# Optimization experiments

Hardware: AMD Instinct MI355X
Metric: run time of the kernel (lower is better)

## Reference

```python
import jax, jax.numpy as jnp
import numpy as np

N, E, G = 30000, 240000, 1000
F, H = 78, 10            # in-features, GAT heads
HID = F * H              # 780
NEG_SLOPE = 0.2


def setup_inputs() -> dict:
    key = jax.random.key(0)
    ks = jax.random.split(key, 12)
    x = jax.random.normal(ks[0], (N, F), dtype=jnp.float32)
    edge_index = jax.random.randint(ks[1], (2, E), 0, N, dtype=jnp.int32)
    batch = jnp.sort(jax.random.randint(ks[2], (N,), 0, G, dtype=jnp.int32))
    def lin(k, fan_in, shape):
        return (jax.random.normal(k, shape, dtype=jnp.float32)
                / jnp.sqrt(jnp.float32(fan_in)))
    return {
        "x": x,
        "edge_index": edge_index,
        "batch": batch,
        "W_gat": lin(ks[3], F, (F, HID)),          # GATConv lin weight
        "att_src": lin(ks[4], F, (H, F)),          # GAT attention vectors
        "att_dst": lin(ks[5], F, (H, F)),
        "b_gat": jnp.zeros((HID,), jnp.float32),
        "W_gcn": lin(ks[6], HID, (HID, HID)),
        "b_gcn": jnp.zeros((HID,), jnp.float32),
        "W1": lin(ks[7], 2 * HID, (2 * HID, 1500)),
        "b1": jnp.zeros((1500,), jnp.float32),
        "W2": lin(ks[8], 1500, (1500, 128)),
        "b2": jnp.zeros((128,), jnp.float32),
    }


def _with_self_loops(edge_index):
    loop = jnp.arange(N, dtype=edge_index.dtype)
    src = jnp.concatenate([edge_index[0], loop])
    dst = jnp.concatenate([edge_index[1], loop])
    return src, dst


def reference(x, edge_index, batch, W_gat, att_src, att_dst, b_gat,
              W_gcn, b_gcn, W1, b1, W2, b2):
    src, dst = _with_self_loops(edge_index)  # [E+N]

    # ---- GATConv(78 -> 78, heads=10, concat) ----
    h = (x @ W_gat).reshape(N, H, F)                       # [N,H,F]
    a_src = jnp.einsum('nhf,hf->nh', h, att_src)           # [N,H]
    a_dst = jnp.einsum('nhf,hf->nh', h, att_dst)
    e = jax.nn.leaky_relu(a_src[src] + a_dst[dst], NEG_SLOPE)  # [Et,H]
    # segment softmax over incoming edges of each dst node
    e_max = jax.ops.segment_max(e, dst, num_segments=N)
    e_exp = jnp.exp(e - e_max[dst])
    denom = jax.ops.segment_sum(e_exp, dst, num_segments=N)
    alpha = e_exp / denom[dst]                             # [Et,H]
    msg = h[src] * alpha[:, :, None]                       # [Et,H,F]
    out = jax.ops.segment_sum(msg, dst, num_segments=N).reshape(N, HID) + b_gat
    out = jax.nn.relu(out)

    # ---- GCNConv(780 -> 780), symmetric norm with self loops ----
    h2 = out @ W_gcn                                       # [N,HID]
    deg = jax.ops.segment_sum(jnp.ones_like(dst, jnp.float32), dst,
                              num_segments=N)
    dinv = jax.lax.rsqrt(jnp.maximum(deg, 1.0))
    norm = dinv[src] * dinv[dst]                           # [Et]
    out2 = jax.ops.segment_sum(norm[:, None] * h2[src], dst,
                               num_segments=N) + b_gcn
    out2 = jax.nn.relu(out2)

    # ---- global mean / max pool over molecules ----
    counts = jax.ops.segment_sum(jnp.ones((N,), jnp.float32), batch,
                                 num_segments=G)
    gsum = jax.ops.segment_sum(out2, batch, num_segments=G)
    gmean = gsum / jnp.maximum(counts, 1.0)[:, None]
    gmax = jax.ops.segment_max(out2, batch, num_segments=G)
    gmax = jnp.where(counts[:, None] > 0, gmax, 0.0)
    pooled = jnp.concatenate([gmean, gmax], axis=1)        # [G, 1560]

    # ---- MLP head (dropout = identity at eval) ----
    hidfc = jax.nn.relu(pooled @ W1 + b1)
    return hidfc @ W2 + b2                                 # [G, 128]
```

## Files before the change

kernel.cpp:

```cpp
#include <hip/hip_runtime.h>

#define NN 30000
#define EE 240000
#define ET 270000
#define GG 1000
#define NH 10
#define FF 78
#define HID 780
#define NEG_SLOPE 0.2f

#define LD_H 784
#define KP_GCN 800
#define NP_HID 896
#define KP_X 96
#define LD_Z 960
#define MP_N 30080
#define KP_P 1600
#define NP_W1 1536
#define LD_FC 1536
#define MP_G 1024

#define MT 128
#define NT 128
#define NBLK 30
#define EB 4

#define C_X   (MP_N * KP_X)
#define C_WE  (NH * 128 * 96)
#define C_WC  (NP_HID * KP_GCN)
#define C_W1  (NP_W1 * KP_P)
#define C_W2  (128 * LD_FC)
#define C_PB  KP_GCN
#define C_WS  (FF * 2 * NH)
#define C_IN  NN
#define C_TOT (C_X + C_WE + C_WC + C_W1 + C_W2 + C_PB + C_WS + C_IN)

typedef __bf16 bf16_8 __attribute__((ext_vector_type(8)));
typedef float f32x4 __attribute__((ext_vector_type(4)));

__device__ __forceinline__ void async_copy16(const void* g, void* l) {
  __builtin_amdgcn_global_load_lds(
      (const __attribute__((address_space(1))) void*)g,
      (__attribute__((address_space(3))) void*)l, 16, 0, 0);
}

__device__ __forceinline__ float bf2f(unsigned int bits) {
  return __uint_as_float(bits << 16);
}

template <bool OUT_BF, int KBC, bool DBUF>
__global__ __launch_bounds__(256) void mfma_gemm(
    const __bf16* __restrict__ A, const __bf16* __restrict__ BT,
    float* __restrict__ Cf, __bf16* __restrict__ Cb,
    const float* __restrict__ bias, int M, int Kp, int Nout, int ldc,
    int relu, int rp, int nct, int mtiles) {
  constexpr int NST = KBC / 32;
  constexpr int TST = KBC / 16;
  constexpr int STAGEB = (KBC / 8) * MT * 8 * 2;
  __shared__ char smem[32768];
  int rt, ct;
  if (rp > 0) {
    int bid = blockIdx.x;
    int p = bid & 7, s = bid >> 3;
    int q = s / nct;
    rt = p * rp + q;
    ct = s - q * nct;
    if (rt >= mtiles) return;
  } else {
    rt = blockIdx.y; ct = blockIdx.x;
  }
  int row0 = rt * MT, col0 = ct * NT;
  int tid = threadIdx.x;
  int lane = tid & 63, wave = tid >> 6;
  int wm = (wave & 1) * 64, wn = (wave >> 1) * 64;
  int l15 = lane & 15, quad = lane >> 4;
  f32x4 acc[4][4] = {};

  auto stage = [&](int k0, int buf) {
    char* baseA = smem + (DBUF ? buf * 2 * STAGEB : 0);
    char* baseB = baseA + STAGEB;
    for (int t = 0; t < TST; t++) {
      int base = t * 256 + wave * 64;
      int s = base + lane;
      int kc = s >> 7, r = s & 127;
      async_copy16(A + (size_t)(row0 + r) * Kp + k0 + kc * 8,
                   baseA + (size_t)base * 16);
    }
    for (int t = 0; t < TST; t++) {
      int base = t * 256 + wave * 64;
      int s = base + lane;
      int kc = s >> 7, r = s & 127;
      async_copy16(BT + (size_t)(col0 + r) * Kp + k0 + kc * 8,
                   baseB + (size_t)base * 16);
    }
  };
  auto compute = [&](int buf) {
    char* baseA = smem + (DBUF ? buf * 2 * STAGEB : 0);
    char* baseB = baseA + STAGEB;
    for (int st = 0; st < NST; st++) {
      bf16_8 af[4], bfv[4];
      for (int mt = 0; mt < 4; mt++)
        af[mt] = *(const bf16_8*)(baseA +
            (size_t)((st * 4 + quad) * MT + wm + mt * 16 + l15) * 16);
      for (int nt = 0; nt < 4; nt++)
        bfv[nt] = *(const bf16_8*)(baseB +
            (size_t)((st * 4 + quad) * MT + wn + nt * 16 + l15) * 16);
      for (int mt = 0; mt < 4; mt++)
        for (int nt = 0; nt < 4; nt++)
          acc[mt][nt] = __builtin_amdgcn_mfma_f32_16x16x32_bf16(
              af[mt], bfv[nt], acc[mt][nt], 0, 0, 0);
    }
  };

  if (DBUF) {
    int niter = Kp / KBC;
    stage(0, 0);
    for (int k = 0; k < niter; k++) {
      __syncthreads();
      if (k + 1 < niter) stage((k + 1) * KBC, (k + 1) & 1);
      compute(k & 1);
    }
    __syncthreads();
  } else {
    for (int k0 = 0; k0 < Kp; k0 += KBC) {
      stage(k0, 0);
      __syncthreads();
      compute(0);
      __syncthreads();
    }
  }

  if (OUT_BF) {
    __bf16* Cs = (__bf16*)smem;
    for (int nt = 0; nt < 4; nt++) {
      int col_l = wn + nt * 16 + l15;
      int gcol = col0 + col_l;
      bool valid = gcol < Nout;
      float bv = (valid && bias) ? bias[gcol] : 0.f;
      int ch = col_l >> 3, wi = col_l & 7;
      for (int mt = 0; mt < 4; mt++) {
        for (int r = 0; r < 4; r++) {
          int rl = wm + mt * 16 + quad * 4 + r;
          float v = 0.f;
          if (valid) {
            v = acc[mt][nt][r] + bv;
            if (relu) v = fmaxf(v, 0.f);
          }
          Cs[rl * 128 + ((ch ^ (rl & 7)) << 3) + wi] = (__bf16)v;
        }
      }
    }
    __syncthreads();
    for (int idx = tid; idx < MT * 16; idx += 256) {
      int rl = idx >> 4, ch = idx & 15;
      int grow = row0 + rl, gcol = col0 + ch * 8;
      if (grow < M && gcol + 8 <= ldc)
        *(bf16_8*)(Cb + (size_t)grow * ldc + gcol) =
            *(const bf16_8*)&Cs[rl * 128 + ((ch ^ (rl & 7)) << 3)];
    }
  } else {
    for (int nt = 0; nt < 4; nt++) {
      int col = col0 + wn + nt * 16 + l15;
      if (col >= ldc) continue;
      bool valid = col < Nout;
      float bv = (valid && bias) ? bias[col] : 0.f;
      for (int mt = 0; mt < 4; mt++) {
        int rbase = row0 + wm + mt * 16 + quad * 4;
        for (int r = 0; r < 4; r++) {
          int row = rbase + r;
          if (row >= M) continue;
          float v = 0.f;
          if (valid) {
            v = acc[mt][nt][r] + bv;
            if (relu) v = fmaxf(v, 0.f);
          }
          Cf[(size_t)row * ldc + col] = v;
        }
      }
    }
  }
}

__global__ __launch_bounds__(256) void gemm_head(
    const __bf16* __restrict__ z, const __bf16* __restrict__ WE,
    const float* __restrict__ pb, __bf16* __restrict__ C) {
  __shared__ char smem[49152];
  __bf16* As = (__bf16*)smem;
  __bf16* Bs = (__bf16*)(smem + 24576);
  int head = blockIdx.x;
  int row0 = blockIdx.y * MT;
  int col0 = 80 * head;
  int tid = threadIdx.x;
  int lane = tid & 63, wave = tid >> 6;
  int wm = (wave & 1) * 64, wn = (wave >> 1) * 64;
  int l15 = lane & 15, quad = lane >> 4;

  for (int t = 0; t < 6; t++) {
    int base = t * 256 + wave * 64;
    int s = base + lane;
    int kc = s >> 7, r = s & 127;
    async_copy16(z + (size_t)(row0 + r) * LD_Z + 96 * head + kc * 8,
                 (char*)As + (size_t)base * 16);
  }
  for (int t = 0; t < 6; t++) {
    int base = t * 256 + wave * 64;
    int s = base + lane;
    int kc = s >> 7, r = s & 127;
    async_copy16(WE + (size_t)head * 128 * 96 + (size_t)r * 96 + kc * 8,
                 (char*)Bs + (size_t)base * 16);
  }
  __syncthreads();

  f32x4 acc[4][4] = {};
  for (int st = 0; st < 3; st++) {
    bf16_8 af[4], bfv[4];
    for (int mt = 0; mt < 4; mt++)
      af[mt] = *(const bf16_8*)&As[(size_t)((st * 4 + quad) * 128 + wm + mt * 16 + l15) * 8];
    for (int nt = 0; nt < 4; nt++)
      bfv[nt] = *(const bf16_8*)&Bs[(size_t)((st * 4 + quad) * 128 + wn + nt * 16 + l15) * 8];
    for (int mt = 0; mt < 4; mt++)
      for (int nt = 0; nt < 4; nt++)
        acc[mt][nt] = __builtin_amdgcn_mfma_f32_16x16x32_bf16(
            af[mt], bfv[nt], acc[mt][nt], 0, 0, 0);
  }
  __syncthreads();

  __bf16* Cs = (__bf16*)smem;
  for (int nt = 0; nt < 4; nt++) {
    int col_l = wn + nt * 16 + l15;
    bool valid = col_l < 78;
    float bv = valid ? pb[col0 + col_l] : 0.f;
    int ch = col_l >> 3, wi = col_l & 7;
    for (int mt = 0; mt < 4; mt++) {
      for (int r = 0; r < 4; r++) {
        int rl = wm + mt * 16 + quad * 4 + r;
        float v = valid ? fmaxf(acc[mt][nt][r] + bv, 0.f) : 0.f;
        Cs[rl * 128 + ((ch ^ (rl & 7)) << 3) + wi] = (__bf16)v;
      }
    }
  }
  __syncthreads();
  for (int idx = tid; idx < MT * 10; idx += 256) {
    int rl = idx / 10, ch = idx - rl * 10;
    int grow = row0 + rl;
    if (grow < NN)
      *(bf16_8*)(C + (size_t)grow * KP_GCN + col0 + ch * 8) =
          *(const bf16_8*)&Cs[rl * 128 + ((ch ^ (rl & 7)) << 3)];
  }
}

__global__ __launch_bounds__(256) void prep_kernel(
    const float* __restrict__ x, const float* __restrict__ W_gat,
    const float* __restrict__ att_src, const float* __restrict__ att_dst,
    const float* __restrict__ W_gcn, const float* __restrict__ W1,
    const float* __restrict__ W2, const float* __restrict__ b_gat,
    __bf16* __restrict__ x_bf, __bf16* __restrict__ WE,
    __bf16* __restrict__ WgcnT, __bf16* __restrict__ W1T,
    __bf16* __restrict__ W2T, float* __restrict__ pb,
    float* __restrict__ wsd, int* __restrict__ cnt, int* __restrict__ fill,
    int* __restrict__ lo, int* __restrict__ hi) {
  int gid = blockIdx.x * 256 + threadIdx.x;
  if (gid < C_X) {
    int n = gid / KP_X, k = gid - n * KP_X;
    x_bf[gid] = (__bf16)((n < NN && k < FF) ? x[(size_t)n * FF + k] : 0.f);
    return;
  }
  gid -= C_X;
  if (gid < C_WE) {
    int h = gid / (128 * 96);
    int rem = gid - h * 128 * 96;
    int n = rem / 96, k = rem - n * 96;
    WE[gid] = (__bf16)((n < FF && k < FF)
                           ? W_gat[(size_t)k * HID + h * FF + n] : 0.f);
    return;
  }
  gid -= C_WE;
  if (gid < C_WC) {
    int n = gid / KP_GCN, kp = gid - n * KP_GCN;
    int hh = kp / 80, f = kp - hh * 80;
    WgcnT[gid] = (__bf16)((n < HID && f < FF)
                              ? W_gcn[(size_t)(FF * hh + f) * HID + n] : 0.f);
    return;
  }
  gid -= C_WC;
  if (gid < C_W1) {
    int n = gid / KP_P, k = gid - n * KP_P;
    W1T[gid] = (__bf16)((n < 1500 && k < 2 * HID) ? W1[(size_t)k * 1500 + n] : 0.f);
    return;
  }
  gid -= C_W1;
  if (gid < C_W2) {
    int n = gid / LD_FC, k = gid - n * LD_FC;
    W2T[gid] = (__bf16)((n < 128 && k < 1500) ? W2[(size_t)k * 128 + n] : 0.f);
    return;
  }
  gid -= C_W2;
  if (gid < C_PB) {
    int hh = gid / 80, f = gid - hh * 80;
    pb[gid] = (f < FF) ? b_gat[FF * hh + f] : 0.f;
    return;
  }
  gid -= C_PB;
  if (gid < C_WS) {
    int k = gid / (2 * NH), c = gid - k * (2 * NH);
    int h = (c < NH) ? c : c - NH;
    const float* att = (c < NH) ? att_src : att_dst;
    float s = 0.f;
    for (int f = 0; f < FF; f++)
      s += W_gat[(size_t)k * HID + h * FF + f] * att[h * FF + f];
    wsd[k * 2 * NH + c] = s;
    return;
  }
  gid -= C_WS;
  if (gid < C_IN) {
    cnt[gid] = 0; fill[gid] = 0;
    if (gid < GG) { lo[gid] = NN; hi[gid] = 0; }
  }
}

__device__ __forceinline__ void edge_sd(const int* __restrict__ ei, int t,
                                        int& s, int& d) {
  if (t < EE) { s = ei[t]; d = ei[EE + t]; }
  else        { s = t - EE; d = t - EE; }
}

__global__ __launch_bounds__(256) void adot_count_kernel(
    const float* __restrict__ x, const float* __restrict__ wsd,
    float* __restrict__ a_src, float* __restrict__ a_dst,
    const int* __restrict__ ei, const int* __restrict__ batch,
    int* __restrict__ cnt, int* __restrict__ lo, int* __restrict__ hi) {
  __shared__ float w_s[FF * 2 * NH];
  for (int i = threadIdx.x; i < FF * 2 * NH; i += 256) w_s[i] = wsd[i];
  int gid = blockIdx.x * 256 + threadIdx.x;
  if (gid < ET) { int s, d; edge_sd(ei, gid, s, d); atomicAdd(&cnt[d], 1); }
  if (gid < NN) {
    int g = batch[gid];
    atomicMin(&lo[g], gid);
    atomicMax(&hi[g], gid + 1);
  }
  __syncthreads();
  if (gid >= NN * 2 * NH) return;
  int n = gid / (2 * NH), c = gid - n * (2 * NH);
  float s = 0.f;
  for (int k = 0; k < FF; k++) s += x[(size_t)n * FF + k] * w_s[k * 2 * NH + c];
  if (c < NH) a_src[n * NH + c] = s;
  else        a_dst[n * NH + (c - NH)] = s;
}

__global__ __launch_bounds__(1024) void scan1_kernel(
    const int* __restrict__ cnt, int* __restrict__ row_ptr,
    int* __restrict__ partial) {
  __shared__ int buf[1024];
  int i = blockIdx.x * 1024 + threadIdx.x;
  int v = (i < NN) ? cnt[i] : 0;
  buf[threadIdx.x] = v;
  __syncthreads();
  for (int off = 1; off < 1024; off <<= 1) {
    int t = (threadIdx.x >= off) ? buf[threadIdx.x - off] : 0;
    __syncthreads();
    buf[threadIdx.x] += t;
    __syncthreads();
  }
  if (i < NN) row_ptr[i] = buf[threadIdx.x] - v;
  if (threadIdx.x == 1023) partial[blockIdx.x] = buf[1023];
}

__global__ __launch_bounds__(256) void scan3_kernel(
    int* __restrict__ row_ptr, const int* __restrict__ partial,
    const int* __restrict__ cnt, float* __restrict__ dinv) {
  __shared__ int pre[NBLK];
  if (threadIdx.x == 0) {
    int run = 0;
    for (int b = 0; b < NBLK; b++) { pre[b] = run; run += partial[b]; }
  }
  __syncthreads();
  int i = blockIdx.x * 256 + threadIdx.x;
  if (i < NN) {
    row_ptr[i] += pre[i >> 10];
    dinv[i] = rsqrtf((float)max(cnt[i], 1));
  }
  if (i == 0) row_ptr[NN] = ET;
}

__global__ void scatter_kernel(const int* __restrict__ ei,
                               const int* __restrict__ row_ptr,
                               int* __restrict__ fill,
                               const float* __restrict__ a_src,
                               const float* __restrict__ a_dst,
                               int* __restrict__ col_src,
                               float* __restrict__ p_csr) {
  int t = blockIdx.x * blockDim.x + threadIdx.x;
  if (t >= ET) return;
  int s, d; edge_sd(ei, t, s, d);
  int pos = row_ptr[d] + atomicAdd(&fill[d], 1);
  col_src[pos] = s;
#pragma unroll
  for (int h = 0; h < NH; h++) {
    float v = a_src[s * NH + h] + a_dst[d * NH + h];
    v = (v > 0.f) ? v : v * NEG_SLOPE;
    p_csr[(size_t)pos * NH + h] = __expf(v);
  }
}

__global__ __launch_bounds__(256) void gat_x_aggr_kernel(
    const int* __restrict__ row_ptr, const int* __restrict__ col_src,
    const float* __restrict__ p_csr, const __bf16* __restrict__ x_bf,
    __bf16* __restrict__ z) {
  int wave = threadIdx.x >> 6;
  int lane = threadIdx.x & 63;
  int d = blockIdx.x * 2 + (wave >> 1);
  int idx = (wave & 1) * 64 + lane;
  int beg = row_ptr[d], end = row_ptr[d + 1];

  if (idx < 100) {
    int h = idx / 10, j = idx - h * 10;
    int k0 = 8 * j;
    float acc[8] = {};
    float sum = 0.f;
    for (int e = beg; e < end; e += EB) {
      int sidx[EB]; float pp[EB];
#pragma unroll
      for (int q = 0; q < EB; q++) {
        bool ok = (e + q < end);
        int ee = ok ? e + q : beg;
        sidx[q] = col_src[ee];
        float p = p_csr[(size_t)ee * NH + h];
        pp[q] = ok ? p : 0.f;
      }
      uint4 rr[EB];
#pragma unroll
      for (int q = 0; q < EB; q++)
        rr[q] = *(const uint4*)(x_bf + (size_t)sidx[q] * KP_X + k0);
#pragma unroll
      for (int q = 0; q < EB; q++) {
        sum += pp[q];
        unsigned int w[4] = {rr[q].x, rr[q].y, rr[q].z, rr[q].w};
#pragma unroll
        for (int k = 0; k < 8; k++) {
          unsigned int bits = (k & 1) ? (w[k >> 1] >> 16) : (w[k >> 1] & 0xffffu);
          acc[k] += bf2f(bits) * pp[q];
        }
      }
    }
    float inv = 1.f / sum;
    bf16_8 o;
#pragma unroll
    for (int k = 0; k < 8; k++) {
      float val = (k0 + k < FF) ? acc[k] * inv : 0.f;
      o[k] = (__bf16)val;
    }
    *(bf16_8*)(z + (size_t)d * LD_Z + 96 * h + k0) = o;
  } else if (idx < 120) {
    int t = idx - 100;
    int h = t >> 1;
    int k0 = 80 + 8 * (t & 1);
    bf16_8 zz = {};
    *(bf16_8*)(z + (size_t)d * LD_Z + 96 * h + k0) = zz;
  }
}

__global__ __launch_bounds__(256) void gcn_aggr_kernel(
    const int* __restrict__ row_ptr, const int* __restrict__ col_src,
    const float* __restrict__ dinv, const __bf16* __restrict__ h2,
    const float* __restrict__ b_gcn, __bf16* __restrict__ out2) {
  int wave = threadIdx.x >> 6;
  int lane = threadIdx.x & 63;
  int d = blockIdx.x * 2 + (wave >> 1);
  int half = wave & 1;
  int beg = row_ptr[d], end = row_ptr[d + 1];
  if (lane >= 49) return;
  int f0 = half * 392 + 8 * lane;
  float dv = dinv[d];
  float acc[8] = {};
  for (int e = beg; e < end; e += EB) {
    int sidx[EB]; float ww[EB];
#pragma unroll
    for (int j = 0; j < EB; j++) {
      bool ok = (e + j < end);
      int ee = ok ? e + j : beg;
      int s = col_src[ee];
      sidx[j] = s;
      ww[j] = ok ? dinv[s] * dv : 0.f;
    }
    uint4 rr[EB];
#pragma unroll
    for (int j = 0; j < EB; j++)
      rr[j] = *(const uint4*)(h2 + (size_t)sidx[j] * LD_H + f0);
#pragma unroll
    for (int j = 0; j < EB; j++) {
      unsigned int wb[4] = {rr[j].x, rr[j].y, rr[j].z, rr[j].w};
#pragma unroll
      for (int k = 0; k < 8; k++) {
        unsigned int bits = (k & 1) ? (wb[k >> 1] >> 16) : (wb[k >> 1] & 0xffffu);
        acc[k] += bf2f(bits) * ww[j];
      }
    }
  }
  bf16_8 o0;
#pragma unroll
  for (int k = 0; k < 8; k++) {
    int f = f0 + k;
    float val = (f < HID) ? fmaxf(acc[k] + b_gcn[f], 0.f) : 0.f;
    o0[k] = (__bf16)val;
  }
  *(bf16_8*)(out2 + (size_t)d * LD_H + f0) = o0;
}

__global__ __launch_bounds__(128) void pool_kernel(
    const __bf16* __restrict__ out2, const int* __restrict__ lo,
    const int* __restrict__ hi, __bf16* __restrict__ pooled) {
  int g = blockIdx.x;
  int l = lo[g], h = hi[g];
  int t = threadIdx.x;
  if (t >= 98) {
    if (t < 103) {
      int base = 1560 + (t - 98) * 8;
      for (int k = 0; k < 8; k++) pooled[(size_t)g * KP_P + base + k] = (__bf16)0.f;
    }
    return;
  }
  int f0 = 8 * t;
  float s[8] = {}, mx[8];
#pragma unroll
  for (int k = 0; k < 8; k++) mx[k] = -1e30f;
  for (int n = l; n < h; n++) {
    uint4 r = *(const uint4*)(out2 + (size_t)n * LD_H + f0);
    unsigned int w[4] = {r.x, r.y, r.z, r.w};
#pragma unroll
    for (int k = 0; k < 8; k++) {
      unsigned int bits = (k & 1) ? (w[k >> 1] >> 16) : (w[k >> 1] & 0xffffu);
      float v = bf2f(bits);
      s[k] += v;
      mx[k] = fmaxf(mx[k], v);
    }
  }
  float invc = (h > l) ? 1.f / (float)(h - l) : 0.f;
#pragma unroll
  for (int k = 0; k < 8; k++) {
    int f = f0 + k;
    if (f >= HID) continue;
    float mean = (h > l) ? s[k] * invc : 0.f;
    float mxx  = (h > l) ? mx[k] : 0.f;
    pooled[(size_t)g * KP_P + f] = (__bf16)mean;
    pooled[(size_t)g * KP_P + HID + f] = (__bf16)mxx;
  }
}

extern "C" void kernel_launch(void* const* d_in, const int* in_sizes, int n_in,
                              void* d_out, int out_size, void* d_ws,
                              size_t ws_size, hipStream_t stream) {
  const float* x        = (const float*)d_in[0];
  const int*   edge_idx = (const int*)d_in[1];
  const int*   batch    = (const int*)d_in[2];
  const float* W_gat    = (const float*)d_in[3];
  const float* att_src  = (const float*)d_in[4];
  const float* att_dst  = (const float*)d_in[5];
  const float* b_gat    = (const float*)d_in[6];
  const float* W_gcn    = (const float*)d_in[7];
  const float* b_gcn    = (const float*)d_in[8];
  const float* W1       = (const float*)d_in[9];
  const float* b1       = (const float*)d_in[10];
  const float* W2       = (const float*)d_in[11];
  const float* b2       = (const float*)d_in[12];
  float* out = (float*)d_out;
  (void)in_sizes; (void)n_in; (void)out_size; (void)ws_size;

  char* ws = (char*)d_ws;
  size_t off = 0;
  auto alloc = [&](size_t bytes) -> void* {
    void* p = ws + off;
    off += (bytes + 255) & ~(size_t)255;
    return p;
  };
  char*  bufR     = (char*)alloc((size_t)MP_N * KP_GCN * 2);
  __bf16* A_bf    = (__bf16*)bufR;
  __bf16* out2b   = (__bf16*)bufR;
  __bf16* z_bf    = (__bf16*)alloc((size_t)MP_N * LD_Z * 2);
  __bf16* h2_bf   = (__bf16*)alloc((size_t)MP_N * LD_H * 2);
  __bf16* x_bf    = (__bf16*)alloc((size_t)MP_N * KP_X * 2);
  __bf16* WE      = (__bf16*)alloc((size_t)NH * 128 * 96 * 2);
  __bf16* WgcnT   = (__bf16*)alloc((size_t)NP_HID * KP_GCN * 2);
  __bf16* W1T     = (__bf16*)alloc((size_t)NP_W1 * KP_P * 2);
  __bf16* W2T     = (__bf16*)alloc((size_t)128 * LD_FC * 2);
  __bf16* pooled  = (__bf16*)alloc((size_t)MP_G * KP_P * 2);
  __bf16* hidfc   = (__bf16*)alloc((size_t)MP_G * LD_FC * 2);
  float* pb       = (float*)alloc((size_t)KP_GCN * 4);
  float* wsd      = (float*)alloc((size_t)FF * 2 * NH * 4);
  float* a_src_b  = (float*)alloc((size_t)NN * NH * 4);
  float* a_dst_b  = (float*)alloc((size_t)NN * NH * 4);
  float* p_csr    = (float*)alloc((size_t)ET * NH * 4);
  int*   cnt      = (int*)alloc((size_t)NN * 4);
  int*   fill     = (int*)alloc((size_t)NN * 4);
  int*   row_ptr  = (int*)alloc((size_t)(NN + 1) * 4);
  int*   col_src  = (int*)alloc((size_t)ET * 4);
  int*   partial  = (int*)alloc((size_t)NBLK * 4);
  int*   lo       = (int*)alloc((size_t)GG * 4);
  int*   hi       = (int*)alloc((size_t)GG * 4);
  float* dinv     = (float*)alloc((size_t)NN * 4);

  prep_kernel<<<(C_TOT + 255) / 256, 256, 0, stream>>>(
      x, W_gat, att_src, att_dst, W_gcn, W1, W2, b_gat, x_bf, WE, WgcnT, W1T,
      W2T, pb, wsd, cnt, fill, lo, hi);

  adot_count_kernel<<<(NN * 2 * NH + 255) / 256, 256, 0, stream>>>(
      x, wsd, a_src_b, a_dst_b, edge_idx, batch, cnt, lo, hi);

  scan1_kernel<<<NBLK, 1024, 0, stream>>>(cnt, row_ptr, partial);
  scan3_kernel<<<(NN + 255) / 256, 256, 0, stream>>>(row_ptr, partial, cnt,
                                                     dinv);
  scatter_kernel<<<(ET + 255) / 256, 256, 0, stream>>>(
      edge_idx, row_ptr, fill, a_src_b, a_dst_b, col_src, p_csr);

  gat_x_aggr_kernel<<<NN / 2, 256, 0, stream>>>(row_ptr, col_src, p_csr, x_bf,
                                                z_bf);
  gemm_head<<<dim3(NH, MP_N / MT), 256, 0, stream>>>(z_bf, WE, pb, A_bf);
  {
    mfma_gemm<true, 32, true><<<dim3(8 * 30 * 7), 256, 0, stream>>>(
        A_bf, WgcnT, nullptr, h2_bf, nullptr, NN, KP_GCN, HID, LD_H, 0,
        30, 7, MP_N / MT);
  }
  gcn_aggr_kernel<<<NN / 2, 256, 0, stream>>>(row_ptr, col_src, dinv, h2_bf,
                                              b_gcn, out2b);

  pool_kernel<<<GG, 128, 0, stream>>>(out2b, lo, hi, pooled);

  {
    dim3 grid(NP_W1 / NT, MP_G / MT);
    mfma_gemm<true, 64, false><<<grid, 256, 0, stream>>>(
        pooled, W1T, nullptr, hidfc, b1, GG, KP_P, 1500, LD_FC, 1, 0, 0, 0);
  }
  {
    dim3 grid(1, MP_G / MT);
    mfma_gemm<false, 64, false><<<grid, 256, 0, stream>>>(
        hidfc, W2T, out, nullptr, b2, GG, LD_FC, 128, 128, 0, 0, 0, 0);
  }
}
```

Before: 537.3 us.

## Use dedicated 256x128-tile GCN GEMM and double-buffer MLP GEMMs

Replaces the generic 128x128 GCN weight GEMM with a 512-thread kernel computing 256x128 tiles with double-buffered async LDS staging, grouped by XCD-style block remapping. Buffers are padded to a multiple of 256 rows so the larger tiles can read without bounds checks. The two MLP head GEMMs switch to the double-buffered template variant, with the LDS size grown to fit. Larger tiles raise operand reuse but use more LDS and registers per block, which can lower occupancy.

```diff
diff --git a/kernel.cpp b/kernel.cpp
--- a/kernel.cpp
+++ b/kernel.cpp
@@ -15,6 +15,7 @@
 #define KP_X 96
 #define LD_Z 960
 #define MP_N 30080
+#define MP_B 30208
 #define KP_P 1600
 #define NP_W1 1536
 #define LD_FC 1536
@@ -57,7 +58,9 @@
   constexpr int NST = KBC / 32;
   constexpr int TST = KBC / 16;
   constexpr int STAGEB = (KBC / 8) * MT * 8 * 2;
-  __shared__ char smem[32768];
+  constexpr int NEED = (DBUF ? 4 : 2) * STAGEB;
+  constexpr int SMEM = NEED > 32768 ? NEED : 32768;
+  __shared__ char smem[SMEM];
   int rt, ct;
   if (rp > 0) {
     int bid = blockIdx.x;
@@ -181,6 +184,78 @@
   }
 }
 
+__global__ __launch_bounds__(512) void gemm_b_kernel(
+    const __bf16* __restrict__ A, const __bf16* __restrict__ BT,
+    __bf16* __restrict__ C) {
+  __shared__ char smem[49152];
+  int bid = blockIdx.x;
+  int p = bid & 7, s = bid >> 3;
+  int q = s / 7;
+  int rt = p * 15 + q;
+  int ct = s - q * 7;
+  if (rt >= MP_B / 256) return;
+  int row0 = rt * 256, col0 = ct * 128;
+  int tid = threadIdx.x;
+  int lane = tid & 63, wave = tid >> 6;
+  int wm = (wave & 3) * 64, wn = (wave >> 2) * 64;
+  int l15 = lane & 15, quad = lane >> 4;
+  f32x4 acc[4][4] = {};
+
+  auto stage = [&](int k0, int buf) {
+    char* baseA = smem + buf * 24576;
+    char* baseB = baseA + 16384;
+    for (int t = 0; t < 2; t++) {
+      int base = t * 512 + wave * 64;
+      int ss = base + lane;
+      int kc = ss >> 8, r = ss & 255;
+      async_copy16(A + (size_t)(row0 + r) * KP_GCN + k0 + kc * 8,
+                   baseA + (size_t)base * 16);
+    }
+    {
+      int base = wave * 64;
+      int ss = base + lane;
+      int kc = ss >> 7, r = ss & 127;
+      async_copy16(BT + (size_t)(col0 + r) * KP_GCN + k0 + kc * 8,
+                   baseB + (size_t)base * 16);
+    }
+  };
+  auto compute = [&](int buf) {
+    char* baseA = smem + buf * 24576;
+    char* baseB = baseA + 16384;
+    bf16_8 af[4], bfv[4];
+    for (int mt = 0; mt < 4; mt++)
+      af[mt] = *(const bf16_8*)(baseA +
+          (size_t)(quad * 256 + wm + mt * 16 + l15) * 16);
+    for (int nt = 0; nt < 4; nt++)
+      bfv[nt] = *(const bf16_8*)(baseB +
+          (size_t)(quad * 128 + wn + nt * 16 + l15) * 16);
+    for (int mt = 0; mt < 4; mt++)
+      for (int nt = 0; nt < 4; nt++)
+        acc[mt][nt] = __builtin_amdgcn_mfma_f32_16x16x32_bf16(
+            af[mt], bfv[nt], acc[mt][nt], 0, 0, 0);
+  };
+
+  constexpr int NITER = KP_GCN / 32;
+  stage(0, 0);
+  for (int k = 0; k < NITER; k++) {
+    __syncthreads();
+    if (k + 1 < NITER) stage((k + 1) * 32, (k + 1) & 1);
+    compute(k & 1);
+  }
+
+  for (int nt = 0; nt < 4; nt++) {
+    int col = col0 + wn + nt * 16 + l15;
+    if (col >= HID) continue;
+    for (int mt = 0; mt < 4; mt++) {
+      int rbase = row0 + wm + mt * 16 + quad * 4;
+      for (int r = 0; r < 4; r++) {
+        int row = rbase + r;
+        if (row < NN) C[(size_t)row * LD_H + col] = (__bf16)acc[mt][nt][r];
+      }
+    }
+  }
+}
+
 __global__ __launch_bounds__(256) void gemm_head(
     const __bf16* __restrict__ z, const __bf16* __restrict__ WE,
     const float* __restrict__ pb, __bf16* __restrict__ C) {
@@ -572,10 +647,10 @@
     off += (bytes + 255) & ~(size_t)255;
     return p;
   };
-  char*  bufR     = (char*)alloc((size_t)MP_N * KP_GCN * 2);
+  char*  bufR     = (char*)alloc((size_t)MP_B * KP_GCN * 2);
   __bf16* A_bf    = (__bf16*)bufR;
   __bf16* out2b   = (__bf16*)bufR;
-  __bf16* z_bf    = (__bf16*)alloc((size_t)MP_N * LD_Z * 2);
+  __bf16* z_bf    = (__bf16*)alloc((size_t)MP_B * LD_Z * 2);
   __bf16* h2_bf   = (__bf16*)alloc((size_t)MP_N * LD_H * 2);
   __bf16* x_bf    = (__bf16*)alloc((size_t)MP_N * KP_X * 2);
   __bf16* WE      = (__bf16*)alloc((size_t)NH * 128 * 96 * 2);
@@ -615,9 +690,7 @@
                                                 z_bf);
   gemm_head<<<dim3(NH, MP_N / MT), 256, 0, stream>>>(z_bf, WE, pb, A_bf);
   {
-    mfma_gemm<true, 32, true><<<dim3(8 * 30 * 7), 256, 0, stream>>>(
-        A_bf, WgcnT, nullptr, h2_bf, nullptr, NN, KP_GCN, HID, LD_H, 0,
-        30, 7, MP_N / MT);
+    gemm_b_kernel<<<dim3(8 * 15 * 7), 512, 0, stream>>>(A_bf, WgcnT, h2_bf);
   }
   gcn_aggr_kernel<<<NN / 2, 256, 0, stream>>>(row_ptr, col_src, dinv, h2_bf,
                                               b_gcn, out2b);
@@ -626,12 +699,12 @@
 
   {
     dim3 grid(NP_W1 / NT, MP_G / MT);
-    mfma_gemm<true, 64, false><<<grid, 256, 0, stream>>>(
+    mfma_gemm<true, 64, true><<<grid, 256, 0, stream>>>(
         pooled, W1T, nullptr, hidfc, b1, GG, KP_P, 1500, LD_FC, 1, 0, 0, 0);
   }
   {
     dim3 grid(1, MP_G / MT);
-    mfma_gemm<false, 64, false><<<grid, 256, 0, stream>>>(
+    mfma_gemm<false, 64, true><<<grid, 256, 0, stream>>>(
         hidfc, W2T, out, nullptr, b2, GG, LD_FC, 128, 128, 0, 0, 0, 0);
   }
 }
```

New measurement: 539.4 us. About the same (+0.4%).
